# Optimization experiments

Hardware: AMD Instinct MI355X
Metric: run time of the kernel (lower is better)

## Reference

```python
import jax, jax.numpy as jnp
import numpy as np

QUALITY = 95
X_MIN, X_MAX = 0.0, 1.0

# JPEG Annex K base quantization tables
_LUMA = np.array([
    [16, 11, 10, 16, 24, 40, 51, 61],
    [12, 12, 14, 19, 26, 58, 60, 55],
    [14, 13, 16, 24, 40, 57, 69, 56],
    [14, 17, 22, 29, 51, 87, 80, 62],
    [18, 22, 37, 56, 68, 109, 103, 77],
    [24, 35, 55, 64, 81, 104, 113, 92],
    [49, 64, 78, 87, 103, 121, 120, 101],
    [72, 92, 95, 98, 112, 100, 103, 99]], dtype=np.float32)
_CHROMA = np.array([
    [17, 18, 24, 47, 99, 99, 99, 99],
    [18, 21, 26, 66, 99, 99, 99, 99],
    [24, 26, 56, 99, 99, 99, 99, 99],
    [47, 66, 99, 99, 99, 99, 99, 99],
    [99, 99, 99, 99, 99, 99, 99, 99],
    [99, 99, 99, 99, 99, 99, 99, 99],
    [99, 99, 99, 99, 99, 99, 99, 99],
    [99, 99, 99, 99, 99, 99, 99, 99]], dtype=np.float32)

def _qtable(base, quality):
    # libjpeg quality scaling (quality >= 50 branch)
    scale = 5000.0 / quality if quality < 50 else 200.0 - 2.0 * quality
    return np.clip(np.floor((base * scale + 50.0) / 100.0), 1.0, 255.0).astype(np.float32)

_QL = jnp.asarray(_qtable(_LUMA, QUALITY))
_QC = jnp.asarray(_qtable(_CHROMA, QUALITY))

# Orthonormal 8x8 DCT-II matrix
_k = np.arange(8)
_D = np.sqrt(2.0 / 8.0) * np.cos((2 * _k[None, :] + 1) * _k[:, None] * np.pi / 16.0)
_D[0, :] /= np.sqrt(2.0)
_D = jnp.asarray(_D.astype(np.float32))

def _jpeg_channel(ch, table):
    """8x8 block DCT -> quantize(round) -> dequantize -> IDCT. ch: [B,H,W] level-shifted."""
    B, H, W = ch.shape
    xb = ch.reshape(B, H // 8, 8, W // 8, 8)
    coef = jnp.einsum('ki,bhiwj,lj->bhkwl', _D, xb, _D)
    t = table[None, None, :, None, :]
    deq = jnp.round(coef / t) * t
    rec = jnp.einsum('ki,bhkwl,lj->bhiwj', _D, deq, _D)
    return rec.reshape(B, H, W)

def _jpeg_roundtrip(x255):
    """x255: [B,H,W,3] float values in [0,255]. Simulates JPEG encode+decode (4:2:0)."""
    r, g, b = x255[..., 0], x255[..., 1], x255[..., 2]
    # JFIF RGB -> YCbCr
    y = 0.299 * r + 0.587 * g + 0.114 * b
    cb = -0.168736 * r - 0.331264 * g + 0.5 * b + 128.0
    cr = 0.5 * r - 0.418688 * g - 0.081312 * b + 128.0
    # Luma at full resolution
    y2 = _jpeg_channel(y - 128.0, _QL) + 128.0
    # Chroma: 2x2 average downsample (4:2:0), codec, nearest upsample
    def down(c):
        B, H, W = c.shape
        return c.reshape(B, H // 2, 2, W // 2, 2).mean(axis=(2, 4))
    def up(c):
        return jnp.repeat(jnp.repeat(c, 2, axis=1), 2, axis=2)
    cb2 = up(_jpeg_channel(down(cb) - 128.0, _QC) + 128.0)
    cr2 = up(_jpeg_channel(down(cr) - 128.0, _QC) + 128.0)
    # YCbCr -> RGB
    r2 = y2 + 1.402 * (cr2 - 128.0)
    g2 = y2 - 0.344136 * (cb2 - 128.0) - 0.714136 * (cr2 - 128.0)
    b2 = y2 + 1.772 * (cb2 - 128.0)
    rgb = jnp.stack([r2, g2, b2], axis=-1)
    return jnp.round(jnp.clip(rgb, 0.0, 255.0))  # decoded uint8 values


def setup_inputs() -> dict:
    key = jax.random.key(0)
    x = jax.random.uniform(key, (32, 512, 512, 3), dtype=jnp.float32)
    return {"x": x}


def reference(x):
    # inputs -> uint8 pixel values (tf.cast truncation; values are >= 0)
    x255 = jnp.clip(jnp.floor((x - X_MIN) / ((X_MAX - X_MIN) / 255.0)), 0.0, 255.0)
    dec = _jpeg_roundtrip(x255)
    # back to input range/dtype
    return dec / (255.0 / (X_MAX - X_MIN)) + X_MIN
```

## Files before the change

### kernel.cpp

```cpp
#include <hip/hip_runtime.h>
#include <cstddef>

static constexpr float D8[8][8] = {
  { 0.35355339059327373f, 0.35355339059327373f, 0.35355339059327373f, 0.35355339059327373f,
    0.35355339059327373f, 0.35355339059327373f, 0.35355339059327373f, 0.35355339059327373f},
  { 0.4903926402016152f,  0.4157348061512726f,  0.27778511650980114f, 0.09754516100806417f,
   -0.09754516100806417f,-0.27778511650980114f,-0.4157348061512726f, -0.4903926402016152f},
  { 0.46193976625564337f, 0.19134171618254492f,-0.19134171618254492f,-0.46193976625564337f,
   -0.46193976625564337f,-0.19134171618254492f, 0.19134171618254492f, 0.46193976625564337f},
  { 0.4157348061512726f, -0.09754516100806417f,-0.4903926402016152f, -0.27778511650980114f,
    0.27778511650980114f, 0.4903926402016152f,  0.09754516100806417f,-0.4157348061512726f},
  { 0.35355339059327373f,-0.35355339059327373f,-0.35355339059327373f, 0.35355339059327373f,
    0.35355339059327373f,-0.35355339059327373f,-0.35355339059327373f, 0.35355339059327373f},
  { 0.27778511650980114f,-0.4903926402016152f,  0.09754516100806417f, 0.4157348061512726f,
   -0.4157348061512726f, -0.09754516100806417f, 0.4903926402016152f, -0.27778511650980114f},
  { 0.19134171618254492f,-0.46193976625564337f, 0.46193976625564337f,-0.19134171618254492f,
   -0.19134171618254492f, 0.46193976625564337f,-0.46193976625564337f, 0.19134171618254492f},
  { 0.09754516100806417f,-0.27778511650980114f, 0.4157348061512726f, -0.4903926402016152f,
    0.4903926402016152f, -0.4157348061512726f,  0.27778511650980114f,-0.09754516100806417f},
};

static constexpr float QLt[8][8] = {
  {2,1,1,2,2,4,5,6},
  {1,1,1,2,3,6,6,6},
  {1,1,2,2,4,6,7,6},
  {1,2,2,3,5,9,8,6},
  {2,2,4,6,7,11,10,8},
  {2,4,6,6,8,10,11,9},
  {5,6,8,9,10,12,12,10},
  {7,9,10,10,11,10,10,10},
};
static constexpr float QCt[8][8] = {
  {2,2,2,5,10,10,10,10},
  {2,2,3,7,10,10,10,10},
  {2,3,6,10,10,10,10,10},
  {5,7,10,10,10,10,10,10},
  {10,10,10,10,10,10,10,10},
  {10,10,10,10,10,10,10,10},
  {10,10,10,10,10,10,10,10},
  {10,10,10,10,10,10,10,10},
};

struct F2 { float q, r; };
struct QTab { F2 v[8][8]; };
static constexpr QTab mkq(const float (&b)[8][8]) {
  QTab t{};
  for (int i = 0; i < 8; ++i)
    for (int j = 0; j < 8; ++j) { t.v[i][j].q = b[i][j]; t.v[i][j].r = 1.0f / b[i][j]; }
  return t;
}
static constexpr QTab QLp = mkq(QLt);
static constexpr QTab QCp = mkq(QCt);

__device__ __forceinline__ void dct8(const float x[8], float u[8]) {
  #pragma unroll
  for (int k = 0; k < 8; ++k) {
    float a = D8[k][0] * x[0];
    #pragma unroll
    for (int j = 1; j < 8; ++j) a += D8[k][j] * x[j];
    u[k] = a;
  }
}
__device__ __forceinline__ void idct8(const float x[8], float u[8]) {
  #pragma unroll
  for (int j = 0; j < 8; ++j) {
    float a = x[0] * D8[0][j];
    #pragma unroll
    for (int m = 1; m < 8; ++m) a += x[m] * D8[m][j];
    u[j] = a;
  }
}

__device__ __forceinline__ float to255(float x) {
  const float c255 = (float)(1.0 / 255.0);
  float y  = x * 255.0f;
  float fl = floorf(y);
  float fr = y - fl;
  if (__builtin_expect(fr < 2e-4f || fr > 1.0f - 2e-4f, 0)) {
    fl = floorf(x / c255);
  }
  return fminf(fmaxf(fl, 0.0f), 255.0f);
}

__device__ __forceinline__ float quant_rt(float u, F2 qp) {
  float tq = u * qp.r;
  float n  = rintf(tq);
  float d  = fabsf(tq - n);
  if (__builtin_expect(d > 0.499f, 0)) {
    n = rintf(u / qp.q);
  }
  return n * qp.q;
}

__global__ __launch_bounds__(128) void jpeg_rt(const float* __restrict__ in,
                                               float* __restrict__ out)
{
  __shared__ __align__(16) float LDSB[2 * 1792];

  const int t   = threadIdx.x;
  const int w   = t >> 6;
  const int l   = t & 63;
  const int tx  = blockIdx.x;
  const int ty  = blockIdx.y;
  const int img = blockIdx.z;

  float* A = LDSB + w * 1792;
  float* B = A + 896;

  const int pr = l >> 3;
  const int pc = l & 7;
  const int colbase = tx*64 + w*32 + 4*pc;

  {
    const size_t r0 = (size_t)img * 512 + (size_t)(ty*16 + 2*pr);
    const float* rp0 = in + (r0*512 + colbase)*3;
    const float* rp1 = rp0 + 512*3;
    float4 L0 = ((const float4*)rp0)[0];
    float4 L1 = ((const float4*)rp0)[1];
    float4 L2 = ((const float4*)rp0)[2];
    float4 L3 = ((const float4*)rp1)[0];
    float4 L4 = ((const float4*)rp1)[1];
    float4 L5 = ((const float4*)rp1)[2];
    float px[2][12] = {{L0.x,L0.y,L0.z,L0.w,L1.x,L1.y,L1.z,L1.w,L2.x,L2.y,L2.z,L2.w},
                       {L3.x,L3.y,L3.z,L3.w,L4.x,L4.y,L4.z,L4.w,L5.x,L5.y,L5.z,L5.w}};
    float yv[2][4], cbv[2][4], crv[2][4];
    #pragma unroll
    for (int rr = 0; rr < 2; ++rr) {
      #pragma unroll
      for (int p = 0; p < 4; ++p) {
        float r = to255(px[rr][3*p+0]);
        float g = to255(px[rr][3*p+1]);
        float b = to255(px[rr][3*p+2]);
        float y  =  0.299f*r + 0.587f*g + 0.114f*b;
        float cb = -0.168736f*r - 0.331264f*g + 0.5f*b + 128.0f;
        float cr =  0.5f*r - 0.418688f*g - 0.081312f*b + 128.0f;
        yv[rr][p]  = y - 128.0f;
        cbv[rr][p] = cb;
        crv[rr][p] = cr;
      }
    }
    *(float4*)&A[(2*pr+0)*36 + 4*pc] = make_float4(yv[0][0],yv[0][1],yv[0][2],yv[0][3]);
    *(float4*)&A[(2*pr+1)*36 + 4*pc] = make_float4(yv[1][0],yv[1][1],yv[1][2],yv[1][3]);
    float cb0 = ((cbv[0][0]+cbv[0][1]) + (cbv[1][0]+cbv[1][1]))*0.25f - 128.0f;
    float cb1 = ((cbv[0][2]+cbv[0][3]) + (cbv[1][2]+cbv[1][3]))*0.25f - 128.0f;
    float cr0 = ((crv[0][0]+crv[0][1]) + (crv[1][0]+crv[1][1]))*0.25f - 128.0f;
    float cr1 = ((crv[0][2]+crv[0][3]) + (crv[1][2]+crv[1][3]))*0.25f - 128.0f;
    *(float2*)&A[576 + pr*20 + 2*pc] = make_float2(cb0, cb1);
    *(float2*)&A[736 + pr*20 + 2*pc] = make_float2(cr0, cr1);
  }

  auto planeAddr = [](int tb, int i) -> int {
    if (tb < 8)  return ((tb >> 2)*8 + i)*36 + (tb & 3)*8;
    if (tb < 10) return 576 + i*20 + (tb - 8)*8;
    return 736 + i*20 + (tb - 10)*8;
  };

  #pragma unroll
  for (int iter = 0; iter < 2; ++iter) {
    const int task = iter*64 + l;
    if (task < 96) {
      const int tb = task >> 3, i = task & 7;
      const float* src = A + planeAddr(tb, i);
      float xr[8], u[8];
      *(float4*)&xr[0] = *(const float4*)&src[0];
      *(float4*)&xr[4] = *(const float4*)&src[4];
      dct8(xr, u);
      *(float4*)&B[tb*68 + i*8 + 0] = make_float4(u[0],u[1],u[2],u[3]);
      *(float4*)&B[tb*68 + i*8 + 4] = make_float4(u[4],u[5],u[6],u[7]);
    }
  }

  #pragma unroll
  for (int iter = 0; iter < 2; ++iter) {
    const int task = iter*64 + l;
    if (task < 96) {
      const int tb = task >> 3, kk = task & 7;
      float s[8], u[8], v[8];
      #pragma unroll
      for (int i = 0; i < 8; ++i) s[i] = B[tb*68 + i*8 + kk];
      dct8(s, u);
      if (tb < 8) {
        #pragma unroll
        for (int m = 0; m < 8; ++m) u[m] = quant_rt(u[m], QLp.v[m][kk]);
      } else {
        #pragma unroll
        for (int m = 0; m < 8; ++m) u[m] = quant_rt(u[m], QCp.v[m][kk]);
      }
      idct8(u, v);
      *(float4*)&A[tb*68 + kk*8 + 0] = make_float4(v[0],v[1],v[2],v[3]);
      *(float4*)&A[tb*68 + kk*8 + 4] = make_float4(v[4],v[5],v[6],v[7]);
    }
  }

  #pragma unroll
  for (int iter = 0; iter < 2; ++iter) {
    const int task = iter*64 + l;
    if (task < 96) {
      const int tb = task >> 3, j = task & 7;
      float wv[8], z[8];
      #pragma unroll
      for (int m = 0; m < 8; ++m) wv[m] = A[tb*68 + m*8 + j];
      idct8(wv, z);
      float* dst = B + planeAddr(tb, j);
      *(float4*)&dst[0] = make_float4(z[0],z[1],z[2],z[3]);
      *(float4*)&dst[4] = make_float4(z[4],z[5],z[6],z[7]);
    }
  }

  {
    const float c255 = (float)(1.0 / 255.0);
    float y0[4], y1[4];
    *(float4*)y0 = *(const float4*)&B[(2*pr+0)*36 + 4*pc];
    *(float4*)y1 = *(const float4*)&B[(2*pr+1)*36 + 4*pc];
    float2 cbp2 = *(const float2*)&B[576 + pr*20 + 2*pc];
    float2 crp2 = *(const float2*)&B[736 + pr*20 + 2*pc];
    float cbq[2] = {cbp2.x, cbp2.y};
    float crq[2] = {crp2.x, crp2.y};
    #pragma unroll
    for (int rr = 0; rr < 2; ++rr) {
      float ov[12];
      #pragma unroll
      for (int p = 0; p < 4; ++p) {
        float y2  = (rr ? y1[p] : y0[p]) + 128.0f;
        float cb2 = cbq[p>>1] + 128.0f;
        float cr2 = crq[p>>1] + 128.0f;
        float r2 = y2 + 1.402f*(cr2 - 128.0f);
        float g2 = y2 - 0.344136f*(cb2 - 128.0f) - 0.714136f*(cr2 - 128.0f);
        float b2 = y2 + 1.772f*(cb2 - 128.0f);
        ov[3*p+0] = rintf(fminf(fmaxf(r2, 0.0f), 255.0f)) * c255;
        ov[3*p+1] = rintf(fminf(fmaxf(g2, 0.0f), 255.0f)) * c255;
        ov[3*p+2] = rintf(fminf(fmaxf(b2, 0.0f), 255.0f)) * c255;
      }
      const size_t grow = (size_t)img * 512 + (size_t)(ty*16 + 2*pr + rr);
      float* op = out + (grow*512 + colbase)*3;
      ((float4*)op)[0] = make_float4(ov[0],ov[1],ov[2],ov[3]);
      ((float4*)op)[1] = make_float4(ov[4],ov[5],ov[6],ov[7]);
      ((float4*)op)[2] = make_float4(ov[8],ov[9],ov[10],ov[11]);
    }
  }
}

extern "C" void kernel_launch(void* const* d_in, const int* in_sizes, int n_in,
                              void* d_out, int out_size, void* d_ws, size_t ws_size,
                              hipStream_t stream) {
  (void)in_sizes; (void)n_in; (void)d_ws; (void)ws_size; (void)out_size;
  const float* x = (const float*)d_in[0];
  float* out = (float*)d_out;
  dim3 grid(8, 32, 32);
  jpeg_rt<<<grid, dim3(128), 0, stream>>>(x, out);
}
```

Measured before the change: 188.9 us.

## Run the DCT stages in place in LDS, split luma/chroma tasks, use double-precision quantisation

The separate A/B LDS buffers become one per-wave buffer that every DCT stage updates in place. This halves shared memory per block, and launch bounds now request 8 blocks per CU to raise occupancy. The task loop is restructured so each lane handles one luma block row and, on the first 32 lanes, one chroma block row, which removes the per-task table branch. The float fast paths for pixel scaling and quantisation, each with a rare fallback to exact division, are replaced by a single double-precision multiply, trading branches for FP64 instructions.

```diff
diff --git a/kernel.cpp b/kernel.cpp
--- a/kernel.cpp
+++ b/kernel.cpp
@@ -41,16 +41,17 @@
   {10,10,10,10,10,10,10,10},
 };
 
-struct F2 { float q, r; };
-struct QTab { F2 v[8][8]; };
-static constexpr QTab mkq(const float (&b)[8][8]) {
-  QTab t{};
+struct QE { double r; float q; float pad; };
+struct QTabE { QE v[8][8]; };
+static constexpr QTabE mkqe(const float (&b)[8][8]) {
+  QTabE t{};
   for (int i = 0; i < 8; ++i)
-    for (int j = 0; j < 8; ++j) { t.v[i][j].q = b[i][j]; t.v[i][j].r = 1.0f / b[i][j]; }
+    for (int j = 0; j < 8; ++j)
+      t.v[i][j] = QE{1.0 / (double)b[i][j], b[i][j], 0.0f};
   return t;
 }
-static constexpr QTab QLp = mkq(QLt);
-static constexpr QTab QCp = mkq(QCt);
+static constexpr QTabE QLe = mkqe(QLt);
+static constexpr QTabE QCe = mkqe(QCt);
 
 __device__ __forceinline__ void dct8(const float x[8], float u[8]) {
   #pragma unroll
@@ -72,30 +73,20 @@
 }
 
 __device__ __forceinline__ float to255(float x) {
-  const float c255 = (float)(1.0 / 255.0);
-  float y  = x * 255.0f;
-  float fl = floorf(y);
-  float fr = y - fl;
-  if (__builtin_expect(fr < 2e-4f || fr > 1.0f - 2e-4f, 0)) {
-    fl = floorf(x / c255);
-  }
-  return fminf(fmaxf(fl, 0.0f), 255.0f);
-}
-
-__device__ __forceinline__ float quant_rt(float u, F2 qp) {
-  float tq = u * qp.r;
-  float n  = rintf(tq);
-  float d  = fabsf(tq - n);
-  if (__builtin_expect(d > 0.499f, 0)) {
-    n = rintf(u / qp.q);
-  }
-  return n * qp.q;
-}
-
-__global__ __launch_bounds__(128) void jpeg_rt(const float* __restrict__ in,
-                                               float* __restrict__ out)
+  constexpr double R = 1.0 / (double)(1.0f / 255.0f);
+  float q = (float)((double)x * R);
+  return fminf(fmaxf(floorf(q), 0.0f), 255.0f);
+}
+
+__device__ __forceinline__ float quant_rt(float u, const QE& e) {
+  float t = (float)((double)u * e.r);
+  return rintf(t) * e.q;
+}
+
+__global__ __launch_bounds__(128, 8) void jpeg_rt(const float* __restrict__ in,
+                                                  float* __restrict__ out)
 {
-  __shared__ __align__(16) float LDSB[2 * 1792];
+  __shared__ __align__(16) float LDSB[2 * 896];
 
   const int t   = threadIdx.x;
   const int w   = t >> 6;
@@ -104,8 +95,7 @@
   const int ty  = blockIdx.y;
   const int img = blockIdx.z;
 
-  float* A = LDSB + w * 1792;
-  float* B = A + 896;
+  float* P = LDSB + w * 896;
 
   const int pr = l >> 3;
   const int pc = l & 7;
@@ -139,14 +129,14 @@
         crv[rr][p] = cr;
       }
     }
-    *(float4*)&A[(2*pr+0)*36 + 4*pc] = make_float4(yv[0][0],yv[0][1],yv[0][2],yv[0][3]);
-    *(float4*)&A[(2*pr+1)*36 + 4*pc] = make_float4(yv[1][0],yv[1][1],yv[1][2],yv[1][3]);
+    *(float4*)&P[(2*pr+0)*36 + 4*pc] = make_float4(yv[0][0],yv[0][1],yv[0][2],yv[0][3]);
+    *(float4*)&P[(2*pr+1)*36 + 4*pc] = make_float4(yv[1][0],yv[1][1],yv[1][2],yv[1][3]);
     float cb0 = ((cbv[0][0]+cbv[0][1]) + (cbv[1][0]+cbv[1][1]))*0.25f - 128.0f;
     float cb1 = ((cbv[0][2]+cbv[0][3]) + (cbv[1][2]+cbv[1][3]))*0.25f - 128.0f;
     float cr0 = ((crv[0][0]+crv[0][1]) + (crv[1][0]+crv[1][1]))*0.25f - 128.0f;
     float cr1 = ((crv[0][2]+crv[0][3]) + (crv[1][2]+crv[1][3]))*0.25f - 128.0f;
-    *(float2*)&A[576 + pr*20 + 2*pc] = make_float2(cb0, cb1);
-    *(float2*)&A[736 + pr*20 + 2*pc] = make_float2(cr0, cr1);
+    *(float2*)&P[576 + pr*20 + 2*pc] = make_float2(cb0, cb1);
+    *(float2*)&P[736 + pr*20 + 2*pc] = make_float2(cr0, cr1);
   }
 
   auto planeAddr = [](int tb, int i) -> int {
@@ -155,65 +145,77 @@
     return 736 + i*20 + (tb - 10)*8;
   };
 
-  #pragma unroll
-  for (int iter = 0; iter < 2; ++iter) {
-    const int task = iter*64 + l;
-    if (task < 96) {
-      const int tb = task >> 3, i = task & 7;
-      const float* src = A + planeAddr(tb, i);
-      float xr[8], u[8];
-      *(float4*)&xr[0] = *(const float4*)&src[0];
-      *(float4*)&xr[4] = *(const float4*)&src[4];
+  const int tb0 = l >> 3;
+  const int tb1 = 8 + (l >> 3);
+  const int ri  = l & 7;
+
+  {
+    float xr[8], u[8];
+    const float* src = P + planeAddr(tb0, ri);
+    *(float4*)&xr[0] = *(const float4*)&src[0];
+    *(float4*)&xr[4] = *(const float4*)&src[4];
+    dct8(xr, u);
+    *(float4*)&P[tb0*68 + ri*8 + 0] = make_float4(u[0],u[1],u[2],u[3]);
+    *(float4*)&P[tb0*68 + ri*8 + 4] = make_float4(u[4],u[5],u[6],u[7]);
+    if (l < 32) {
+      const float* src1 = P + planeAddr(tb1, ri);
+      *(float4*)&xr[0] = *(const float4*)&src1[0];
+      *(float4*)&xr[4] = *(const float4*)&src1[4];
       dct8(xr, u);
-      *(float4*)&B[tb*68 + i*8 + 0] = make_float4(u[0],u[1],u[2],u[3]);
-      *(float4*)&B[tb*68 + i*8 + 4] = make_float4(u[4],u[5],u[6],u[7]);
-    }
-  }
-
-  #pragma unroll
-  for (int iter = 0; iter < 2; ++iter) {
-    const int task = iter*64 + l;
-    if (task < 96) {
-      const int tb = task >> 3, kk = task & 7;
-      float s[8], u[8], v[8];
-      #pragma unroll
-      for (int i = 0; i < 8; ++i) s[i] = B[tb*68 + i*8 + kk];
+      *(float4*)&P[tb1*68 + ri*8 + 0] = make_float4(u[0],u[1],u[2],u[3]);
+      *(float4*)&P[tb1*68 + ri*8 + 4] = make_float4(u[4],u[5],u[6],u[7]);
+    }
+  }
+
+  {
+    float s[8], u[8], v[8];
+    #pragma unroll
+    for (int i = 0; i < 8; ++i) s[i] = P[tb0*68 + i*8 + ri];
+    dct8(s, u);
+    #pragma unroll
+    for (int m = 0; m < 8; ++m) u[m] = quant_rt(u[m], QLe.v[m][ri]);
+    idct8(u, v);
+    *(float4*)&P[tb0*68 + ri*8 + 0] = make_float4(v[0],v[1],v[2],v[3]);
+    *(float4*)&P[tb0*68 + ri*8 + 4] = make_float4(v[4],v[5],v[6],v[7]);
+    if (l < 32) {
+      #pragma unroll
+      for (int i = 0; i < 8; ++i) s[i] = P[tb1*68 + i*8 + ri];
       dct8(s, u);
-      if (tb < 8) {
-        #pragma unroll
-        for (int m = 0; m < 8; ++m) u[m] = quant_rt(u[m], QLp.v[m][kk]);
-      } else {
-        #pragma unroll
-        for (int m = 0; m < 8; ++m) u[m] = quant_rt(u[m], QCp.v[m][kk]);
-      }
+      #pragma unroll
+      for (int m = 0; m < 8; ++m) u[m] = quant_rt(u[m], QCe.v[m][ri]);
       idct8(u, v);
-      *(float4*)&A[tb*68 + kk*8 + 0] = make_float4(v[0],v[1],v[2],v[3]);
-      *(float4*)&A[tb*68 + kk*8 + 4] = make_float4(v[4],v[5],v[6],v[7]);
-    }
-  }
-
-  #pragma unroll
-  for (int iter = 0; iter < 2; ++iter) {
-    const int task = iter*64 + l;
-    if (task < 96) {
-      const int tb = task >> 3, j = task & 7;
-      float wv[8], z[8];
-      #pragma unroll
-      for (int m = 0; m < 8; ++m) wv[m] = A[tb*68 + m*8 + j];
-      idct8(wv, z);
-      float* dst = B + planeAddr(tb, j);
-      *(float4*)&dst[0] = make_float4(z[0],z[1],z[2],z[3]);
-      *(float4*)&dst[4] = make_float4(z[4],z[5],z[6],z[7]);
+      *(float4*)&P[tb1*68 + ri*8 + 0] = make_float4(v[0],v[1],v[2],v[3]);
+      *(float4*)&P[tb1*68 + ri*8 + 4] = make_float4(v[4],v[5],v[6],v[7]);
+    }
+  }
+
+  {
+    float w0[8], w1[8], z[8];
+    #pragma unroll
+    for (int m = 0; m < 8; ++m) w0[m] = P[tb0*68 + m*8 + ri];
+    if (l < 32) {
+      #pragma unroll
+      for (int m = 0; m < 8; ++m) w1[m] = P[tb1*68 + m*8 + ri];
+    }
+    idct8(w0, z);
+    float* dst = P + planeAddr(tb0, ri);
+    *(float4*)&dst[0] = make_float4(z[0],z[1],z[2],z[3]);
+    *(float4*)&dst[4] = make_float4(z[4],z[5],z[6],z[7]);
+    if (l < 32) {
+      idct8(w1, z);
+      float* dst1 = P + planeAddr(tb1, ri);
+      *(float4*)&dst1[0] = make_float4(z[0],z[1],z[2],z[3]);
+      *(float4*)&dst1[4] = make_float4(z[4],z[5],z[6],z[7]);
     }
   }
 
   {
     const float c255 = (float)(1.0 / 255.0);
     float y0[4], y1[4];
-    *(float4*)y0 = *(const float4*)&B[(2*pr+0)*36 + 4*pc];
-    *(float4*)y1 = *(const float4*)&B[(2*pr+1)*36 + 4*pc];
-    float2 cbp2 = *(const float2*)&B[576 + pr*20 + 2*pc];
-    float2 crp2 = *(const float2*)&B[736 + pr*20 + 2*pc];
+    *(float4*)y0 = *(const float4*)&P[(2*pr+0)*36 + 4*pc];
+    *(float4*)y1 = *(const float4*)&P[(2*pr+1)*36 + 4*pc];
+    float2 cbp2 = *(const float2*)&P[576 + pr*20 + 2*pc];
+    float2 crp2 = *(const float2*)&P[736 + pr*20 + 2*pc];
     float cbq[2] = {cbp2.x, cbp2.y};
     float crq[2] = {crp2.x, crp2.y};
     #pragma unroll
```

Result: no change. 186.2 us (-1.4%).
